# Kernel tuning notes

Hardware: AMD Instinct MI355X
Metric: run time of the kernel (lower is better)

The kernel has to match this reference:

```python
import jax, jax.numpy as jnp
import numpy as np

R = 8
EPS = 1e-08

def _diff_x(c, r):
    # c: (..., H, W), summed along H (axis -2)
    left = c[..., r:2 * r + 1, :]
    middle = c[..., 2 * r + 1:, :] - c[..., :-2 * r - 1, :]
    right = c[..., -1:, :] - c[..., -2 * r - 1:-r - 1, :]
    return jnp.concatenate([left, middle, right], axis=-2)

def _diff_y(c, r):
    left = c[..., :, r:2 * r + 1]
    middle = c[..., :, 2 * r + 1:] - c[..., :, :-2 * r - 1]
    right = c[..., :, -1:] - c[..., :, -2 * r - 1:-r - 1]
    return jnp.concatenate([left, middle, right], axis=-1)

def boxfilter(x, r):
    # summed-area-table box sum over the last two axes
    return _diff_y(_diff_x(jnp.cumsum(x, axis=-2), r).cumsum(axis=-1), r)

def setup_inputs() -> dict:
    key = jax.random.key(0)
    k1, k2 = jax.random.split(key)
    n, t, c, h, w = 4, 8, 3, 512, 512
    inp = jax.random.uniform(k1, (n, t, c, h, w), dtype=jnp.float32)
    ref = jax.random.uniform(k2, (n, t, c, h, w), dtype=jnp.float32)
    return {"input": inp, "ref": ref}

def reference(input, ref):
    n, t, c, h, w = input.shape
    assert h > 2 * R + 1 and w > 2 * R + 1
    # NOTE: faithful to the original: y = input (ref is only shape-checked)
    x = input.reshape(n * t, c, h, w)  # vectorize the per-timestep loop
    N = boxfilter(jnp.ones((1, 1, h, w), dtype=input.dtype), R)  # window counts
    mean_x = boxfilter(x, R) / N
    mean_y = mean_x  # y == x in original code
    cov_xy = boxfilter(x * x, R) / N - mean_x * mean_y
    var_x = boxfilter(x * x, R) / N - mean_x * mean_x
    A = cov_xy / (var_x + EPS)
    b = mean_y - A * mean_x
    mean_A = boxfilter(A, R) / N
    mean_b = boxfilter(b, R) / N
    out = mean_A * x + mean_b
    return out.reshape(n, t, c, h, w)
```

## Files before the change

kernel.cpp:

```cpp
#include <hip/hip_runtime.h>


#define RR   8
#define DD   17
#define WW   512
#define HH   512
#define BHH  32
#define NT   128
#define CPT  4
#define PADW (WW + 2*RR)
#define FEPS 1e-8f

union F4 { float4 v; float f[4]; };

__device__ __forceinline__ float frcp(float a) { return __builtin_amdgcn_rcpf(a); }

__device__ __forceinline__ void stage1(const float* __restrict__ lsum1,
                                       const float* __restrict__ lsum2,
                                       int j, int c0, const float* inv_nx,
                                       F4& Af, F4& Bf)
{
    float w1[CPT + 16], w2[CPT + 16];
#pragma unroll
    for (int q = 0; q < 5; ++q) {
        F4 t1, t2;
        t1.v = *(const float4*)&lsum1[c0 + 4 * q];
        t2.v = *(const float4*)&lsum2[c0 + 4 * q];
#pragma unroll
        for (int e = 0; e < 4; ++e) { w1[4*q+e] = t1.f[e]; w2[4*q+e] = t2.f[e]; }
    }
    float S1[CPT], S2[CPT];
    float s1 = 0.f, s2 = 0.f;
#pragma unroll
    for (int q = 0; q < DD; ++q) { s1 += w1[q]; s2 += w2[q]; }
    S1[0] = s1; S2[0] = s2;
#pragma unroll
    for (int k = 1; k < CPT; ++k) {
        S1[k] = S1[k-1] - w1[k-1] + w1[k-1+DD];
        S2[k] = S2[k-1] - w2[k-1] + w2[k-1+DD];
    }
    const int   ny    = min(HH - 1, j + RR) - max(0, j - RR) + 1;
    const float invny = frcp((float)ny);
#pragma unroll
    for (int k = 0; k < CPT; ++k) {
        float invN = invny * inv_nx[k];
        float mean = S1[k] * invN;
        float ex2  = S2[k] * invN;
        float var  = ex2 - mean * mean;
        float A    = var * frcp(var + FEPS);
        Af.f[k] = A;
        Bf.f[k] = mean - A * mean;
    }
}

__global__ __launch_bounds__(NT, 3) void gf_kernel(
    const float* __restrict__ x, float* __restrict__ out)
{
    __shared__ float lv1[PADW], lv2[PADW];
    __shared__ float ld1[PADW], ld2[PADW];
    __shared__ float lva[PADW], lvb[PADW];

    const int tid = threadIdx.x;
    const int img = blockIdx.y;
    const int r0  = blockIdx.x * BHH;
    const float* px = x   + (size_t)img * (HH * WW);
    float*       po = out + (size_t)img * (HH * WW);
    const int c0 = tid * CPT;

    if (tid < RR) {
        lv1[tid] = 0.f; lv2[tid] = 0.f; ld1[tid] = 0.f; ld2[tid] = 0.f;
        lva[tid] = 0.f; lvb[tid] = 0.f;
        lv1[RR+WW+tid] = 0.f; lv2[RR+WW+tid] = 0.f;
        ld1[RR+WW+tid] = 0.f; ld2[RR+WW+tid] = 0.f;
        lva[RR+WW+tid] = 0.f; lvb[RR+WW+tid] = 0.f;
    }

    float inv_nx[CPT];
#pragma unroll
    for (int k = 0; k < CPT; ++k) {
        int c  = c0 + k;
        int nx = min(WW - 1, c + RR) - max(0, c - RR) + 1;
        inv_nx[k] = frcp((float)nx);
    }

    float v1[CPT]  = {0,0,0,0}, v2[CPT]  = {0,0,0,0};
    float v1d[CPT] = {0,0,0,0}, v2d[CPT] = {0,0,0,0};
    float va[CPT]  = {0,0,0,0}, vb[CPT]  = {0,0,0,0};

    const int rstart  = max(0, r0 - 2 * RR);
    const int rstart2 = max(0, r0 - RR);
    const int i2max   = r0 + BHH - 1;
    const int i1max   = min(HH - 1, i2max + RR);
    const int rend    = i2max + 2 * RR;

    F4 xr_cur; xr_cur.v = make_float4(0,0,0,0);
    if (rstart < HH) xr_cur.v = *(const float4*)(px + (size_t)rstart * WW + c0);

#pragma unroll 1
    for (int r = rstart; r <= rend; ++r) {
        const int  i1   = r - RR;
        const int  jd   = i1 - DD;
        const int  i2   = r - 2 * RR;
        const bool addV  = (r < HH);
        const bool subV  = (r - DD >= rstart);
        const bool subVd = (r - 2*DD >= rstart);
        const bool addA  = (i1 >= rstart2) && (i1 <= i1max);
        const bool subA  = (jd >= rstart2);
        const bool st2   = (i2 >= r0);

        const int rn = r + 1;
        F4 xr_nxt; xr_nxt.v = xr_cur.v;
        if (rn < HH && rn <= rend)
            xr_nxt.v = *(const float4*)(px + (size_t)rn * WW + c0);
        F4 xm, xdd, xi;
        if (subV)  xm.v  = *(const float4*)(px + (size_t)(r - DD)  * WW + c0);
        if (subVd) xdd.v = *(const float4*)(px + (size_t)(r - 2*DD)* WW + c0);
        if (st2)   xi.v  = *(const float4*)(px + (size_t)i2 * WW + c0);

#pragma unroll
        for (int k = 0; k < CPT; ++k) {
            if (addV)  { v1[k]  += xr_cur.f[k]; v2[k]  += xr_cur.f[k] * xr_cur.f[k]; }
            if (subV)  { v1[k]  -= xm.f[k];     v2[k]  -= xm.f[k] * xm.f[k]; }
            if (subV)  { v1d[k] += xm.f[k];     v2d[k] += xm.f[k] * xm.f[k]; }
            if (subVd) { v1d[k] -= xdd.f[k];    v2d[k] -= xdd.f[k] * xdd.f[k]; }
        }
        {
            F4 a, b, c, d;
#pragma unroll
            for (int k = 0; k < CPT; ++k) { a.f[k] = v1[k]; b.f[k] = v2[k]; c.f[k] = v1d[k]; d.f[k] = v2d[k]; }
            *(float4*)&lv1[RR + c0] = a.v;
            *(float4*)&lv2[RR + c0] = b.v;
            *(float4*)&ld1[RR + c0] = c.v;
            *(float4*)&ld2[RR + c0] = d.v;
        }
        __syncthreads();

        if (addA) {
            F4 Af, Bf;
            stage1(lv1, lv2, i1, c0, inv_nx, Af, Bf);
#pragma unroll
            for (int k = 0; k < CPT; ++k) { va[k] += Af.f[k]; vb[k] += Bf.f[k]; }
        }
        if (subA) {
            F4 Af, Bf;
            stage1(ld1, ld2, jd, c0, inv_nx, Af, Bf);
#pragma unroll
            for (int k = 0; k < CPT; ++k) { va[k] -= Af.f[k]; vb[k] -= Bf.f[k]; }
        }
        if (st2) {
            F4 a, b;
#pragma unroll
            for (int k = 0; k < CPT; ++k) { a.f[k] = va[k]; b.f[k] = vb[k]; }
            *(float4*)&lva[RR + c0] = a.v;
            *(float4*)&lvb[RR + c0] = b.v;
        }
        __syncthreads();

        if (st2) {
            float wa[CPT + 16], wb[CPT + 16];
#pragma unroll
            for (int q = 0; q < 5; ++q) {
                F4 t1, t2;
                t1.v = *(const float4*)&lva[c0 + 4 * q];
                t2.v = *(const float4*)&lvb[c0 + 4 * q];
#pragma unroll
                for (int e = 0; e < 4; ++e) { wa[4*q+e] = t1.f[e]; wb[4*q+e] = t2.f[e]; }
            }
            float SA[CPT], SB[CPT];
            float sa = 0.f, sb = 0.f;
#pragma unroll
            for (int q = 0; q < DD; ++q) { sa += wa[q]; sb += wb[q]; }
            SA[0] = sa; SB[0] = sb;
#pragma unroll
            for (int k = 1; k < CPT; ++k) {
                SA[k] = SA[k-1] - wa[k-1] + wa[k-1+DD];
                SB[k] = SB[k-1] - wb[k-1] + wb[k-1+DD];
            }
            const int   ny2   = min(HH - 1, i2 + RR) - max(0, i2 - RR) + 1;
            const float invny = frcp((float)ny2);
            F4 of;
#pragma unroll
            for (int k = 0; k < CPT; ++k) {
                float invN = invny * inv_nx[k];
                of.f[k] = (SA[k] * invN) * xi.f[k] + SB[k] * invN;
            }
            *(float4*)(po + (size_t)i2 * WW + c0) = of.v;
        }

        xr_cur.v = xr_nxt.v;
    }
}

extern "C" void kernel_launch(void* const* d_in, const int* in_sizes, int n_in,
                              void* d_out, int out_size, void* d_ws, size_t ws_size,
                              hipStream_t stream) {
    const float* x  = (const float*)d_in[0];
    float* out      = (float*)d_out;
    const int nimg  = in_sizes[0] / (HH * WW);
    dim3 grid(HH / BHH, nimg);
    gf_kernel<<<grid, NT, 0, stream>>>(x, out);
}
```

Measured before the change: 276.0 us.

## Use single-wave blocks with 8 columns per thread and split even/odd LDS layout

Shrinks each block to one 64-thread wavefront handling 8 columns per thread, so the two __syncthreads per row become lgkmcnt waits plus scheduling barriers. The LDS buffers become even/odd float4 halves with one-slot zero padding so each thread reads its 24-wide horizontal window in six float4 loads. The subtract-row loads for xm and xdd are now prefetched one iteration ahead like the add row. This trades barrier cost for fewer threads per block and higher register pressure, with occupancy hinted at 2.

Result: no change. 275.0 us (-0.4%).

```diff
diff --git a/kernel.cpp b/kernel.cpp
--- a/kernel.cpp
+++ b/kernel.cpp
@@ -6,29 +6,42 @@
 #define WW   512
 #define HH   512
 #define BHH  32
-#define NT   128
-#define CPT  4
-#define PADW (WW + 2*RR)
+#define NT   64
+#define CPT  8
+#define NSLOT 66
 #define FEPS 1e-8f
 
 union F4 { float4 v; float f[4]; };
 
 __device__ __forceinline__ float frcp(float a) { return __builtin_amdgcn_rcpf(a); }
 
-__device__ __forceinline__ void stage1(const float* __restrict__ lsum1,
-                                       const float* __restrict__ lsum2,
-                                       int j, int c0, const float* inv_nx,
-                                       F4& Af, F4& Bf)
+#define LFENCE() do { asm volatile("s_waitcnt lgkmcnt(0)" ::: "memory"); \
+                      __builtin_amdgcn_sched_barrier(0); } while (0)
+
+__device__ __forceinline__ void hwin(const float4* __restrict__ ev,
+                                     const float4* __restrict__ od,
+                                     int l, float* w)
 {
-    float w1[CPT + 16], w2[CPT + 16];
-#pragma unroll
-    for (int q = 0; q < 5; ++q) {
-        F4 t1, t2;
-        t1.v = *(const float4*)&lsum1[c0 + 4 * q];
-        t2.v = *(const float4*)&lsum2[c0 + 4 * q];
-#pragma unroll
-        for (int e = 0; e < 4; ++e) { w1[4*q+e] = t1.f[e]; w2[4*q+e] = t2.f[e]; }
-    }
+    F4 a, b, c, d, e, g;
+    a.v = ev[l];     b.v = od[l];
+    c.v = ev[l + 1]; d.v = od[l + 1];
+    e.v = ev[l + 2]; g.v = od[l + 2];
+#pragma unroll
+    for (int t = 0; t < 4; ++t) {
+        w[t]      = a.f[t]; w[4 + t]  = b.f[t];
+        w[8 + t]  = c.f[t]; w[12 + t] = d.f[t];
+        w[16 + t] = e.f[t]; w[20 + t] = g.f[t];
+    }
+}
+
+__device__ __forceinline__ void stage1(const float4* ev1, const float4* od1,
+                                       const float4* ev2, const float4* od2,
+                                       int j, int l, const float* inv_nx,
+                                       float* Af, float* Bf)
+{
+    float w1[24], w2[24];
+    hwin(ev1, od1, l, w1);
+    hwin(ev2, od2, l, w2);
     float S1[CPT], S2[CPT];
     float s1 = 0.f, s2 = 0.f;
 #pragma unroll
@@ -48,31 +61,31 @@
         float ex2  = S2[k] * invN;
         float var  = ex2 - mean * mean;
         float A    = var * frcp(var + FEPS);
-        Af.f[k] = A;
-        Bf.f[k] = mean - A * mean;
-    }
-}
-
-__global__ __launch_bounds__(NT, 3) void gf_kernel(
+        Af[k] = A;
+        Bf[k] = mean - A * mean;
+    }
+}
+
+__global__ __launch_bounds__(NT, 2) void gf_kernel(
     const float* __restrict__ x, float* __restrict__ out)
 {
-    __shared__ float lv1[PADW], lv2[PADW];
-    __shared__ float ld1[PADW], ld2[PADW];
-    __shared__ float lva[PADW], lvb[PADW];
-
-    const int tid = threadIdx.x;
+    __shared__ float4 EV[6][NSLOT];
+    __shared__ float4 OD[6][NSLOT];
+
+    const int l   = threadIdx.x;
     const int img = blockIdx.y;
     const int r0  = blockIdx.x * BHH;
     const float* px = x   + (size_t)img * (HH * WW);
     float*       po = out + (size_t)img * (HH * WW);
-    const int c0 = tid * CPT;
-
-    if (tid < RR) {
-        lv1[tid] = 0.f; lv2[tid] = 0.f; ld1[tid] = 0.f; ld2[tid] = 0.f;
-        lva[tid] = 0.f; lvb[tid] = 0.f;
-        lv1[RR+WW+tid] = 0.f; lv2[RR+WW+tid] = 0.f;
-        ld1[RR+WW+tid] = 0.f; ld2[RR+WW+tid] = 0.f;
-        lva[RR+WW+tid] = 0.f; lvb[RR+WW+tid] = 0.f;
+    const int c0 = l * CPT;
+
+    if (l < 24) {
+        const int buf = l >> 2, s = l & 3;
+        const float4 z = make_float4(0.f, 0.f, 0.f, 0.f);
+        if      (s == 0) EV[buf][0]         = z;
+        else if (s == 1) OD[buf][0]         = z;
+        else if (s == 2) EV[buf][NSLOT - 1] = z;
+        else             OD[buf][NSLOT - 1] = z;
     }
 
     float inv_nx[CPT];
@@ -83,9 +96,9 @@
         inv_nx[k] = frcp((float)nx);
     }
 
-    float v1[CPT]  = {0,0,0,0}, v2[CPT]  = {0,0,0,0};
-    float v1d[CPT] = {0,0,0,0}, v2d[CPT] = {0,0,0,0};
-    float va[CPT]  = {0,0,0,0}, vb[CPT]  = {0,0,0,0};
+    float v1[CPT]  = {0,0,0,0,0,0,0,0}, v2[CPT]  = {0,0,0,0,0,0,0,0};
+    float v1d[CPT] = {0,0,0,0,0,0,0,0}, v2d[CPT] = {0,0,0,0,0,0,0,0};
+    float va[CPT]  = {0,0,0,0,0,0,0,0}, vb[CPT]  = {0,0,0,0,0,0,0,0};
 
     const int rstart  = max(0, r0 - 2 * RR);
     const int rstart2 = max(0, r0 - RR);
@@ -93,79 +106,125 @@
     const int i1max   = min(HH - 1, i2max + RR);
     const int rend    = i2max + 2 * RR;
 
-    F4 xr_cur; xr_cur.v = make_float4(0,0,0,0);
-    if (rstart < HH) xr_cur.v = *(const float4*)(px + (size_t)rstart * WW + c0);
+    F4 xr_c[2], xm_c[2], xdd_c[2];
+#pragma unroll
+    for (int h = 0; h < 2; ++h) {
+        xr_c[h].v = make_float4(0,0,0,0);
+        xm_c[h].v = make_float4(0,0,0,0);
+        xdd_c[h].v = make_float4(0,0,0,0);
+    }
+    {
+        const float* p = px + (size_t)rstart * WW + c0;
+        xr_c[0].v = *(const float4*)(p);
+        xr_c[1].v = *(const float4*)(p + 4);
+    }
 
 #pragma unroll 1
     for (int r = rstart; r <= rend; ++r) {
-        const int  i1   = r - RR;
-        const int  jd   = i1 - DD;
-        const int  i2   = r - 2 * RR;
+        const int  i1    = r - RR;
+        const int  jd    = i1 - DD;
+        const int  i2    = r - 2 * RR;
         const bool addV  = (r < HH);
-        const bool subV  = (r - DD >= rstart);
+        const bool subV  = (r - DD   >= rstart);
         const bool subVd = (r - 2*DD >= rstart);
         const bool addA  = (i1 >= rstart2) && (i1 <= i1max);
         const bool subA  = (jd >= rstart2);
         const bool st2   = (i2 >= r0);
 
         const int rn = r + 1;
-        F4 xr_nxt; xr_nxt.v = xr_cur.v;
-        if (rn < HH && rn <= rend)
-            xr_nxt.v = *(const float4*)(px + (size_t)rn * WW + c0);
-        F4 xm, xdd, xi;
-        if (subV)  xm.v  = *(const float4*)(px + (size_t)(r - DD)  * WW + c0);
-        if (subVd) xdd.v = *(const float4*)(px + (size_t)(r - 2*DD)* WW + c0);
-        if (st2)   xi.v  = *(const float4*)(px + (size_t)i2 * WW + c0);
+        F4 xr_n[2] = {xr_c[0], xr_c[1]};
+        F4 xm_n[2] = {xm_c[0], xm_c[1]};
+        F4 xdd_n[2] = {xdd_c[0], xdd_c[1]};
+        if (rn < HH && rn <= rend) {
+            const float* p = px + (size_t)rn * WW + c0;
+            xr_n[0].v = *(const float4*)(p); xr_n[1].v = *(const float4*)(p + 4);
+        }
+        if (rn - DD >= rstart && rn <= rend) {
+            const float* p = px + (size_t)(rn - DD) * WW + c0;
+            xm_n[0].v = *(const float4*)(p); xm_n[1].v = *(const float4*)(p + 4);
+        }
+        if (rn - 2*DD >= rstart && rn <= rend) {
+            const float* p = px + (size_t)(rn - 2*DD) * WW + c0;
+            xdd_n[0].v = *(const float4*)(p); xdd_n[1].v = *(const float4*)(p + 4);
+        }
+        F4 xi[2];
+        if (st2) {
+            const float* p = px + (size_t)i2 * WW + c0;
+            xi[0].v = *(const float4*)(p); xi[1].v = *(const float4*)(p + 4);
+        }
 
 #pragma unroll
         for (int k = 0; k < CPT; ++k) {
-            if (addV)  { v1[k]  += xr_cur.f[k]; v2[k]  += xr_cur.f[k] * xr_cur.f[k]; }
-            if (subV)  { v1[k]  -= xm.f[k];     v2[k]  -= xm.f[k] * xm.f[k]; }
-            if (subV)  { v1d[k] += xm.f[k];     v2d[k] += xm.f[k] * xm.f[k]; }
-            if (subVd) { v1d[k] -= xdd.f[k];    v2d[k] -= xdd.f[k] * xdd.f[k]; }
+            const float xa = xr_c[k >> 2].f[k & 3];
+            const float xb = xm_c[k >> 2].f[k & 3];
+            const float xc = xdd_c[k >> 2].f[k & 3];
+            if (addV)  { v1[k]  += xa; v2[k]  += xa * xa; }
+            if (subV)  { v1[k]  -= xb; v2[k]  -= xb * xb; }
+            if (subV)  { v1d[k] += xb; v2d[k] += xb * xb; }
+            if (subVd) { v1d[k] -= xc; v2d[k] -= xc * xc; }
         }
         {
-            F4 a, b, c, d;
-#pragma unroll
-            for (int k = 0; k < CPT; ++k) { a.f[k] = v1[k]; b.f[k] = v2[k]; c.f[k] = v1d[k]; d.f[k] = v2d[k]; }
-            *(float4*)&lv1[RR + c0] = a.v;
-            *(float4*)&lv2[RR + c0] = b.v;
-            *(float4*)&ld1[RR + c0] = c.v;
-            *(float4*)&ld2[RR + c0] = d.v;
-        }
-        __syncthreads();
+            F4 t;
+#pragma unroll
+            for (int e = 0; e < 4; ++e) t.f[e] = v1[e];
+            EV[0][1 + l] = t.v;
+#pragma unroll
+            for (int e = 0; e < 4; ++e) t.f[e] = v1[4 + e];
+            OD[0][1 + l] = t.v;
+#pragma unroll
+            for (int e = 0; e < 4; ++e) t.f[e] = v2[e];
+            EV[1][1 + l] = t.v;
+#pragma unroll
+            for (int e = 0; e < 4; ++e) t.f[e] = v2[4 + e];
+            OD[1][1 + l] = t.v;
+#pragma unroll
+            for (int e = 0; e < 4; ++e) t.f[e] = v1d[e];
+            EV[2][1 + l] = t.v;
+#pragma unroll
+            for (int e = 0; e < 4; ++e) t.f[e] = v1d[4 + e];
+            OD[2][1 + l] = t.v;
+#pragma unroll
+            for (int e = 0; e < 4; ++e) t.f[e] = v2d[e];
+            EV[3][1 + l] = t.v;
+#pragma unroll
+            for (int e = 0; e < 4; ++e) t.f[e] = v2d[4 + e];
+            OD[3][1 + l] = t.v;
+        }
+        LFENCE();
 
         if (addA) {
-            F4 Af, Bf;
-            stage1(lv1, lv2, i1, c0, inv_nx, Af, Bf);
-#pragma unroll
-            for (int k = 0; k < CPT; ++k) { va[k] += Af.f[k]; vb[k] += Bf.f[k]; }
+            float Af[CPT], Bf[CPT];
+            stage1(EV[0], OD[0], EV[1], OD[1], i1, l, inv_nx, Af, Bf);
+#pragma unroll
+            for (int k = 0; k < CPT; ++k) { va[k] += Af[k]; vb[k] += Bf[k]; }
         }
         if (subA) {
-            F4 Af, Bf;
-            stage1(ld1, ld2, jd, c0, inv_nx, Af, Bf);
-#pragma unroll
-            for (int k = 0; k < CPT; ++k) { va[k] -= Af.f[k]; vb[k] -= Bf.f[k]; }
+            float Af[CPT], Bf[CPT];
+            stage1(EV[2], OD[2], EV[3], OD[3], jd, l, inv_nx, Af, Bf);
+#pragma unroll
+            for (int k = 0; k < CPT; ++k) { va[k] -= Af[k]; vb[k] -= Bf[k]; }
         }
         if (st2) {
-            F4 a, b;
-#pragma unroll
-            for (int k = 0; k < CPT; ++k) { a.f[k] = va[k]; b.f[k] = vb[k]; }
-            *(float4*)&lva[RR + c0] = a.v;
-            *(float4*)&lvb[RR + c0] = b.v;
-        }
-        __syncthreads();
+            F4 t;
+#pragma unroll
+            for (int e = 0; e < 4; ++e) t.f[e] = va[e];
+            EV[4][1 + l] = t.v;
+#pragma unroll
+            for (int e = 0; e < 4; ++e) t.f[e] = va[4 + e];
+            OD[4][1 + l] = t.v;
+#pragma unroll
+            for (int e = 0; e < 4; ++e) t.f[e] = vb[e];
+            EV[5][1 + l] = t.v;
+#pragma unroll
+            for (int e = 0; e < 4; ++e) t.f[e] = vb[4 + e];
+            OD[5][1 + l] = t.v;
+        }
+        LFENCE();
 
         if (st2) {
-            float wa[CPT + 16], wb[CPT + 16];
-#pragma unroll
-            for (int q = 0; q < 5; ++q) {
-                F4 t1, t2;
-                t1.v = *(const float4*)&lva[c0 + 4 * q];
-                t2.v = *(const float4*)&lvb[c0 + 4 * q];
-#pragma unroll
-                for (int e = 0; e < 4; ++e) { wa[4*q+e] = t1.f[e]; wb[4*q+e] = t2.f[e]; }
-            }
+            float wa[24], wb[24];
+            hwin(EV[4], OD[4], l, wa);
+            hwin(EV[5], OD[5], l, wb);
             float SA[CPT], SB[CPT];
             float sa = 0.f, sb = 0.f;
 #pragma unroll
@@ -178,16 +237,21 @@
             }
             const int   ny2   = min(HH - 1, i2 + RR) - max(0, i2 - RR) + 1;
             const float invny = frcp((float)ny2);
-            F4 of;
+            F4 o0, o1;
 #pragma unroll
             for (int k = 0; k < CPT; ++k) {
                 float invN = invny * inv_nx[k];
-                of.f[k] = (SA[k] * invN) * xi.f[k] + SB[k] * invN;
+                float ov   = (SA[k] * invN) * xi[k >> 2].f[k & 3] + SB[k] * invN;
+                if (k < 4) o0.f[k] = ov; else o1.f[k - 4] = ov;
             }
-            *(float4*)(po + (size_t)i2 * WW + c0) = of.v;
-        }
-
-        xr_cur.v = xr_nxt.v;
+            float* p = po + (size_t)i2 * WW + c0;
+            *(float4*)(p)     = o0.v;
+            *(float4*)(p + 4) = o1.v;
+        }
+
+        xr_c[0] = xr_n[0];  xr_c[1] = xr_n[1];
+        xm_c[0] = xm_n[0];  xm_c[1] = xm_n[1];
+        xdd_c[0] = xdd_n[0]; xdd_c[1] = xdd_n[1];
     }
 }
 
```
